# Optimization experiments

Hardware: AMD Instinct MI355X
Metric: run time of the kernel (lower is better)

## Reference

```python
import jax, jax.numpy as jnp
import numpy as np
jax.config.update("jax_enable_x64", True)

N_FFT = 512; HOP = 128; WIN = 512
LAMBDA = 2e-4      # lambda_reg (diagonal loading)
TAPS = 20          # n_frames_past
FCP_EPS = 1e-3     # fcp_epsilon


def _sqrt_hann():
    n = jnp.arange(WIN, dtype=jnp.float32)
    return jnp.sqrt(0.5 * (1.0 - jnp.cos(2.0 * jnp.pi * n / WIN)))


def _stft(x):
    # x: [B, L] float32 -> [B, n_freq, n_frames] complex64 (center=True, constant pad)
    w = _sqrt_hann()
    pad = N_FFT // 2
    xp = jnp.pad(x, ((0, 0), (pad, pad)))
    n_frames = 1 + (xp.shape[-1] - N_FFT) // HOP
    idx = jnp.arange(n_frames)[:, None] * HOP + jnp.arange(N_FFT)[None, :]
    frames = xp[:, idx] * w                      # [B, n_frames, n_fft]
    return jnp.swapaxes(jnp.fft.rfft(frames, axis=-1), -1, -2)


def _istft(spec):
    # spec: [B, n_freq, n_frames] -> [B, (n_frames-1)*HOP]  (torch.istft semantics)
    w = _sqrt_hann()
    frames = jnp.fft.irfft(jnp.swapaxes(spec, -1, -2), n=N_FFT, axis=-1) * w
    n_frames = frames.shape[1]
    Lout = (n_frames - 1) * HOP + N_FFT
    idx = jnp.arange(n_frames)[:, None] * HOP + jnp.arange(N_FFT)[None, :]
    y = jnp.zeros((frames.shape[0], Lout), frames.dtype).at[:, idx].add(frames)
    env = jnp.zeros((Lout,), frames.dtype).at[idx].add(jnp.broadcast_to(w * w, idx.shape))
    y = y / jnp.where(env > 1e-11, env, 1.0)
    pad = N_FFT // 2
    return y[:, pad:Lout - pad]


def _fcp_forward(ref_channel, mixture):
    bs, n_spk, L0 = ref_channel.shape
    n_ch = mixture.shape[1]
    ref = jnp.pad(ref_channel, ((0, 0), (0, 0), (0, N_FFT)))
    mix = jnp.pad(mixture, ((0, 0), (0, 0), (0, N_FFT)))
    sph = _stft(ref.reshape(bs * n_spk, -1))
    mxs = _stft(mix.reshape(bs * n_ch, -1))
    F_, T = sph.shape[-2], sph.shape[-1]
    sph = sph.reshape(bs, n_spk, F_, T).transpose(0, 2, 1, 3)   # [b,f,s,t]
    mxs = mxs.reshape(bs, n_ch, F_, T).transpose(0, 2, 1, 3)    # [b,f,c,t]
    # inverse power weight (fcp_weight_type=0): per (b,f,t), averaged over mics
    power = jnp.mean(mxs.real ** 2 + mxs.imag ** 2, axis=2)     # [b,f,t]
    mx = jnp.max(power, axis=(1, 2), keepdims=True)             # [b,1,1]
    inv_pow = 1.0 / (power + mx * FCP_EPS + 1e-6)               # [b,f,t]
    # Toeplitz stack: Yt[b,f,s,t,p] = sph[b,f,s, t-(TAPS-1)+p] (zero-padded past)
    padded = jnp.pad(sph, ((0, 0), (0, 0), (0, 0), (TAPS - 1, 0)))
    tidx = jnp.arange(TAPS)[:, None] + jnp.arange(T)[None, :]   # [taps, T]
    Yt = jnp.moveaxis(padded[..., tidx], -2, -1)                # [b,f,s,t,taps]
    wYt = Yt * inv_pow[:, :, None, :, None]                     # weighted copy
    R = jnp.einsum('bfstp,bfstq->bfspq', wYt, Yt.conj()) / T    # [b,f,s,taps,taps]
    P = jnp.einsum('bfstp,bfct->bfspc', wYt, mxs.conj()) / T    # [b,f,s,taps,c]
    eye = jnp.eye(TAPS, dtype=jnp.complex128)
    G = jnp.linalg.solve(R.astype(jnp.complex128) + LAMBDA * eye,
                         P.astype(jnp.complex128)).astype(Yt.dtype)
    ret = jnp.einsum('bfstp,bfspc->bfstc', Yt, G.conj())        # [b,f,s,t,c]
    spec_hat = ret.transpose(0, 2, 4, 1, 3).reshape(bs * n_spk * n_ch, F_, T)
    audio = _istft(spec_hat).reshape(bs, n_spk, n_ch, -1)[..., :L0]
    return G.conj(), audio


def setup_inputs():
    key = jax.random.key(0)
    k1, k2 = jax.random.split(key)
    ref_channel = jax.random.normal(k1, (4, 2, 64000), dtype=jnp.float32)
    mixture = jax.random.normal(k2, (4, 6, 64000), dtype=jnp.float32)
    return {"ref_channel": ref_channel, "mixture": mixture}


def reference(ref_channel, mixture):
    return _fcp_forward(ref_channel, mixture)
```

## Files before the change

### kernel.cpp

```cpp
#include <hip/hip_runtime.h>
#include <math.h>

namespace {

constexpr int NB = 4, NSPK = 2, NCHN = 6;
constexpr int LSIG = 64000;
constexpr int NFFT = 512, HOPSZ = 128, NFREQ = 257;
constexpr int NT = 505;
constexpr int TAPS = 20;
constexpr int NG = NB * NFREQ * NSPK;
constexpr int NSIG = NB * NSPK * NCHN;
constexpr float PI_F = 3.14159265358979323846f;
constexpr double LAMBDA_REG = 2e-4;
constexpr float FCP_EPS_F = 1e-3f;
constexpr int G_ELEMS = NG * TAPS * NCHN;
constexpr int NCH4 = (NT + 3) / 4;
constexpr int YPAD_N = TAPS + 2 + NT;
constexpr int NR_TILES = 55;
constexpr int NP_THREADS = 60;

constexpr size_t WS_ALIGN = 256;
constexpr size_t align_up(size_t x) { return (x + WS_ALIGN - 1) & ~(WS_ALIGN - 1); }

constexpr size_t SPH_B  = 0;
constexpr size_t SPH_SZ = (size_t)NB * NSPK * NFREQ * NT * 8;
constexpr size_t SPHT_B = align_up(SPH_B + SPH_SZ);
constexpr size_t MXS_B  = align_up(SPHT_B + SPH_SZ);
constexpr size_t MXS_SZ = (size_t)NB * NCHN * NFREQ * NT * 8;
constexpr size_t POW_B  = align_up(MXS_B + MXS_SZ);
constexpr size_t POW_SZ = (size_t)NB * NFREQ * NT * 4;
constexpr size_t MX_B   = align_up(POW_B + POW_SZ);
constexpr size_t R_B    = align_up(MX_B + (size_t)NB * 4);
constexpr size_t R_SZ   = (size_t)NG * TAPS * TAPS * 8;
constexpr size_t P_B    = align_up(R_B + R_SZ);
constexpr size_t P_SZ   = (size_t)NG * TAPS * NCHN * 8;
constexpr size_t GCT_B  = align_up(P_B + P_SZ);
constexpr size_t GCT_SZ = (size_t)NB * NSPK * TAPS * NCHN * NFREQ * 8;
constexpr size_t FRM_B  = align_up(GCT_B + GCT_SZ);

__device__ __forceinline__ int rev9(int n) { return (int)(__brev((unsigned)n) >> 23); }

__device__ __forceinline__ void fft512_quad(float2* buf, int tid, float sign) {
#pragma unroll
  for (int s = 1; s <= 9; ++s) {
    int half = 1 << (s - 1);
    int blk = tid >> (s - 1);
    int pos = tid & (half - 1);
    int i0 = (blk << s) + pos;
    int i1 = i0 + half;
    float ang = sign * 2.0f * PI_F * (float)pos / (float)(half << 1);
    float sn, cs;
    __sincosf(ang, &sn, &cs);
#pragma unroll
    for (int j = 0; j < 4; ++j) {
      float2 u = buf[j * NFFT + i0], v = buf[j * NFFT + i1];
      float2 vw = make_float2(v.x * cs - v.y * sn, v.x * sn + v.y * cs);
      buf[j * NFFT + i0] = make_float2(u.x + vw.x, u.y + vw.y);
      buf[j * NFFT + i1] = make_float2(u.x - vw.x, u.y - vw.y);
    }
    __syncthreads();
  }
}

__global__ void stft_kernel(const float* __restrict__ ref, const float* __restrict__ mix,
                            float2* __restrict__ sph, float2* __restrict__ spht,
                            float2* __restrict__ mxs) {
  __shared__ float2 buf[4 * NFFT];
  int blk = blockIdx.x;
  int sig = blk / NCH4;
  int ch = blk - sig * NCH4;
  int t0 = ch * 4;
  int nv = min(4, NT - t0);
  int tid = threadIdx.x;
  bool is_ref = sig < NB * NSPK;
  int m = is_ref ? sig : (sig - NB * NSPK);
  const float* src = is_ref ? (ref + (size_t)m * LSIG) : (mix + (size_t)m * LSIG);

  for (int n = tid; n < NFFT; n += 256) {
    float w = __sinf(PI_F * (float)n / (float)NFFT);
    int r = rev9(n);
    int g0 = t0 * HOPSZ + n - NFFT / 2;
#pragma unroll
    for (int j = 0; j < 4; ++j) {
      int gg = g0 + j * HOPSZ;
      float v = (j < nv && gg >= 0 && gg < LSIG) ? src[gg] : 0.0f;
      buf[j * NFFT + r] = make_float2(v * w, 0.0f);
    }
  }
  __syncthreads();
  fft512_quad(buf, tid, -1.0f);

  if (is_ref) {
    float2* d1 = sph + (size_t)m * NFREQ * NT;
    float2* d2 = spht + ((size_t)m * NT + t0) * NFREQ;
    for (int f = tid; f < NFREQ; f += 256) {
#pragma unroll
      for (int j = 0; j < 4; ++j) {
        if (j < nv) {
          float2 v = buf[j * NFFT + f];
          d1[(size_t)f * NT + t0 + j] = v;
          d2[(size_t)j * NFREQ + f] = v;
        }
      }
    }
  } else {
    float2* d1 = mxs + (size_t)m * NFREQ * NT;
    for (int f = tid; f < NFREQ; f += 256) {
#pragma unroll
      for (int j = 0; j < 4; ++j)
        if (j < nv) d1[(size_t)f * NT + t0 + j] = buf[j * NFFT + f];
    }
  }
}

__global__ void power_kernel(const float2* __restrict__ mxs, float* __restrict__ power) {
  int i = blockIdx.x * 256 + threadIdx.x;
  if (i >= NB * NFREQ * NT) return;
  int b = i / (NFREQ * NT);
  int r = i - b * (NFREQ * NT);
  float acc = 0.0f;
#pragma unroll
  for (int c = 0; c < NCHN; ++c) {
    float2 v = mxs[(size_t)(b * NCHN + c) * NFREQ * NT + r];
    acc += v.x * v.x + v.y * v.y;
  }
  power[i] = acc * (1.0f / (float)NCHN);
}

__global__ void max_kernel(const float* __restrict__ power, float* __restrict__ mx) {
  int b = blockIdx.x;
  const float* p = power + (size_t)b * NFREQ * NT;
  float m = 0.0f;
  for (int i = threadIdx.x; i < NFREQ * NT; i += 256) m = fmaxf(m, p[i]);
#pragma unroll
  for (int off = 32; off > 0; off >>= 1) m = fmaxf(m, __shfl_down(m, off, 64));
  __shared__ float sm[4];
  int wave = threadIdx.x >> 6, lane = threadIdx.x & 63;
  if (lane == 0) sm[wave] = m;
  __syncthreads();
  if (threadIdx.x == 0) mx[b] = fmaxf(fmaxf(sm[0], sm[1]), fmaxf(sm[2], sm[3]));
}

__global__ void rp_kernel(const float2* __restrict__ sph, const float2* __restrict__ mxs,
                          const float* __restrict__ power, const float* __restrict__ mx,
                          float2* __restrict__ R, float2* __restrict__ P) {
  __shared__ float2 Ypad[YPAD_N];
  __shared__ float2 MWsh[NCHN][NT];
  __shared__ float Wsh[NT];
  int g = blockIdx.x;
  int s = g & 1;
  int bf = g >> 1;
  int f = bf % NFREQ;
  int b = bf / NFREQ;
  int tid = threadIdx.x;

  const float2* yrow = sph + ((size_t)(b * NSPK + s) * NFREQ + f) * NT;
  const float* prow = power + ((size_t)b * NFREQ + f) * NT;
  float add = mx[b] * FCP_EPS_F + 1e-6f;
  for (int t = tid; t < NT; t += 512) Wsh[t] = 1.0f / (prow[t] + add);
  for (int i = tid; i < YPAD_N; i += 512) {
    bool in = (i >= TAPS - 1) && (i < TAPS - 1 + NT);
    Ypad[i] = in ? yrow[i - (TAPS - 1)] : make_float2(0.0f, 0.0f);
  }
  __syncthreads();
  for (int i = tid; i < NCHN * NT; i += 512) {
    int c = i / NT, t = i - c * NT;
    float2 m = mxs[((size_t)(b * NCHN + c) * NFREQ + f) * NT + t];
    float w = Wsh[t];
    MWsh[c][t] = make_float2(w * m.x, -w * m.y);
  }
  __syncthreads();

  const float invT = 1.0f / (float)NT;
  const int TQ[5] = {0, 126, 252, 378, NT};
  int wave = tid >> 6;
  int lane = tid & 63;
  bool isR = (wave < 4) && (lane < NR_TILES);
  bool isP = (wave >= 4) && (lane < NP_THREADS);

  float x00 = 0.f, y00 = 0.f, x01 = 0.f, y01 = 0.f;
  float x10 = 0.f, y10 = 0.f, x11 = 0.f, y11 = 0.f;
  int pb = 0, qb = 0, pc = 0;

  if (isR) {
    int seg = wave;
    int tlo = TQ[seg], thi = TQ[seg + 1];
    int I = (int)((sqrtf(8.0f * (float)lane + 1.0f) - 1.0f) * 0.5f);
    while ((I + 1) * (I + 2) / 2 <= lane) ++I;
    while (I * (I + 1) / 2 > lane) --I;
    int J = lane - I * (I + 1) / 2;
    pb = 2 * I; qb = 2 * J;
    float2 a0 = Ypad[pb + tlo], a1 = Ypad[pb + tlo + 1];
    float2 b0 = Ypad[qb + tlo], b1 = Ypad[qb + tlo + 1];
    for (int t = tlo; t < thi; ++t) {
      float w = Wsh[t];
      float wax0 = w * a0.x, way0 = w * a0.y;
      float wax1 = w * a1.x, way1 = w * a1.y;
      x00 = fmaf(wax0, b0.x, fmaf(way0, b0.y, x00));
      y00 = fmaf(way0, b0.x, fmaf(-wax0, b0.y, y00));
      x01 = fmaf(wax0, b1.x, fmaf(way0, b1.y, x01));
      y01 = fmaf(way0, b1.x, fmaf(-wax0, b1.y, y01));
      x10 = fmaf(wax1, b0.x, fmaf(way1, b0.y, x10));
      y10 = fmaf(way1, b0.x, fmaf(-wax1, b0.y, y10));
      x11 = fmaf(wax1, b1.x, fmaf(way1, b1.y, x11));
      y11 = fmaf(way1, b1.x, fmaf(-wax1, b1.y, y11));
      a0 = a1; a1 = Ypad[pb + 2 + t];
      b0 = b1; b1 = Ypad[qb + 2 + t];
    }
  } else if (isP) {
    int seg = wave - 4;
    int tlo = TQ[seg], thi = TQ[seg + 1];
    int ih = lane / NCHN;
    pc = lane - ih * NCHN;
    pb = 2 * ih;
    float2 a0 = Ypad[pb + tlo], a1 = Ypad[pb + tlo + 1];
    const float2* MW = &MWsh[pc][0];
    for (int t = tlo; t < thi; ++t) {
      float2 mw = MW[t];
      x00 += a0.x * mw.x - a0.y * mw.y;
      y00 += a0.x * mw.y + a0.y * mw.x;
      x10 += a1.x * mw.x - a1.y * mw.y;
      y10 += a1.x * mw.y + a1.y * mw.x;
      a0 = a1; a1 = Ypad[pb + 2 + t];
    }
  }
  __syncthreads();

  float* scratch = (float*)MWsh;
  if (isR && wave >= 1) {
    float* d = scratch + ((wave - 1) * NR_TILES + lane) * 8;
    d[0] = x00; d[1] = y00; d[2] = x01; d[3] = y01;
    d[4] = x10; d[5] = y10; d[6] = x11; d[7] = y11;
  }
  if (isP && wave >= 5) {
    float* d = scratch + 3 * NR_TILES * 8 + ((wave - 5) * NP_THREADS + lane) * 4;
    d[0] = x00; d[1] = y00; d[2] = x10; d[3] = y10;
  }
  __syncthreads();

  if (isR && wave == 0) {
#pragma unroll
    for (int sgi = 0; sgi < 3; ++sgi) {
      const float* d = scratch + (sgi * NR_TILES + lane) * 8;
      x00 += d[0]; y00 += d[1]; x01 += d[2]; y01 += d[3];
      x10 += d[4]; y10 += d[5]; x11 += d[6]; y11 += d[7];
    }
    float2* Rg = R + (size_t)g * TAPS * TAPS;
#define STORE_R(p_, q_, xx, yy)                                       \
    if ((p_) >= (q_)) {                                                \
      float rx = (xx) * invT, ry = (yy) * invT;                        \
      Rg[(p_) * TAPS + (q_)] = make_float2(rx, ry);                    \
      if ((p_) != (q_)) Rg[(q_) * TAPS + (p_)] = make_float2(rx, -ry); \
    }
    STORE_R(pb, qb, x00, y00)
    STORE_R(pb, qb + 1, x01, y01)
    STORE_R(pb + 1, qb, x10, y10)
    STORE_R(pb + 1, qb + 1, x11, y11)
#undef STORE_R
  }
  if (isP && wave == 4) {
#pragma unroll
    for (int sgi = 0; sgi < 3; ++sgi) {
      const float* d = scratch + 3 * NR_TILES * 8 + (sgi * NP_THREADS + lane) * 4;
      x00 += d[0]; y00 += d[1]; x10 += d[2]; y10 += d[3];
    }
    float2* Pg = P + (size_t)g * TAPS * NCHN;
    Pg[pb * NCHN + pc] = make_float2(x00 * invT, y00 * invT);
    Pg[(pb + 1) * NCHN + pc] = make_float2(x10 * invT, y10 * invT);
  }
}

__global__ void solve_kernel(const float2* __restrict__ R, const float2* __restrict__ P,
                             float* __restrict__ gout, float2* __restrict__ gct) {
  __shared__ double2 A[TAPS][TAPS];
  __shared__ double2 Bm[TAPS][NCHN];
  int g = blockIdx.x;
  int tid = threadIdx.x;
  int s = g & 1;
  int bf = g >> 1;
  int f = bf % NFREQ;
  int b = bf / NFREQ;
  int bs = b * NSPK + s;

  for (int i = tid; i < TAPS * TAPS; i += 64) {
    float2 r = R[(size_t)g * TAPS * TAPS + i];
    A[i / TAPS][i % TAPS] = make_double2((double)r.x, (double)r.y);
  }
  for (int i = tid; i < TAPS * NCHN; i += 64) {
    float2 p = P[(size_t)g * TAPS * NCHN + i];
    Bm[i / NCHN][i % NCHN] = make_double2((double)p.x, (double)p.y);
  }
  __syncthreads();
  if (tid < TAPS) A[tid][tid].x += LAMBDA_REG;
  __syncthreads();

  for (int k = 0; k < TAPS; ++k) {
    if (tid == 0) A[k][k].x = sqrt(A[k][k].x);
    __syncthreads();
    double d = A[k][k].x;
    if (tid > k && tid < TAPS) {
      A[tid][k].x /= d;
      A[tid][k].y /= d;
    }
    __syncthreads();
    int w = TAPS - 1 - k;
    for (int idx = tid; idx < w * w; idx += 64) {
      int i = k + 1 + idx / w;
      int j = k + 1 + idx % w;
      if (i >= j) {
        double2 a = A[i][k], bb = A[j][k];
        A[i][j].x -= a.x * bb.x + a.y * bb.y;
        A[i][j].y -= a.y * bb.x - a.x * bb.y;
      }
    }
    __syncthreads();
  }

  if (tid < NCHN) {
    int c = tid;
    for (int k = 0; k < TAPS; ++k) {
      double sx = Bm[k][c].x, sy = Bm[k][c].y;
      for (int j = 0; j < k; ++j) {
        double2 l = A[k][j], y = Bm[j][c];
        sx -= l.x * y.x - l.y * y.y;
        sy -= l.x * y.y + l.y * y.x;
      }
      double d = A[k][k].x;
      Bm[k][c] = make_double2(sx / d, sy / d);
    }
    for (int k = TAPS - 1; k >= 0; --k) {
      double sx = Bm[k][c].x, sy = Bm[k][c].y;
      for (int j = k + 1; j < TAPS; ++j) {
        double2 l = A[j][k], xv = Bm[j][c];
        sx -= l.x * xv.x + l.y * xv.y;
        sy -= l.x * xv.y - l.y * xv.x;
      }
      double d = A[k][k].x;
      Bm[k][c] = make_double2(sx / d, sy / d);
    }
  }
  __syncthreads();

  for (int i = tid; i < TAPS * NCHN; i += 64) {
    int p = i / NCHN, c = i - p * NCHN;
    double2 gv = Bm[p][c];
    float gx = (float)gv.x, gy = (float)(-gv.y);
    gout[(size_t)g * TAPS * NCHN + i] = gx;
    gct[(((size_t)bs * TAPS + p) * NCHN + c) * NFREQ + f] = make_float2(gx, gy);
  }
}

__global__ void ret_ifft_kernel(const float2* __restrict__ spht, const float2* __restrict__ gct,
                                float* __restrict__ frames) {
  __shared__ float2 buf[4 * NFFT];
  constexpr int NBLK = NSIG * NCH4;
  int bid = blockIdx.x;
  int blk = (bid & 7) * (NBLK / 8) + (bid >> 3);
  int ch = blk % NCH4;
  int sc = blk / NCH4;
  int t0 = ch * 4;
  int nv = min(4, NT - t0);
  int c = sc % NCHN;
  int bs = sc / NCHN;
  int tid = threadIdx.x;

  const float2* gbase = gct + ((size_t)bs * TAPS * NCHN + c) * NFREQ;
  const float2* ysig = spht + (size_t)bs * NT * NFREQ;
  for (int f = tid; f < NFREQ; f += 256) {
    float sx0 = 0.f, sy0 = 0.f, sx1 = 0.f, sy1 = 0.f;
    float sx2 = 0.f, sy2 = 0.f, sx3 = 0.f, sy3 = 0.f;
    float2 g1p = make_float2(0.f, 0.f), g2p = make_float2(0.f, 0.f),
           g3p = make_float2(0.f, 0.f);
#pragma unroll
    for (int k = 0; k <= TAPS + 2; ++k) {
      int u = t0 - (TAPS - 1) + k;
      float2 y = (u >= 0 && u < NT) ? ysig[(size_t)u * NFREQ + f] : make_float2(0.f, 0.f);
      float2 gc = (k < TAPS) ? gbase[(size_t)k * NCHN * NFREQ + f] : make_float2(0.f, 0.f);
      sx0 += y.x * gc.x - y.y * gc.y;   sy0 += y.x * gc.y + y.y * gc.x;
      sx1 += y.x * g1p.x - y.y * g1p.y; sy1 += y.x * g1p.y + y.y * g1p.x;
      sx2 += y.x * g2p.x - y.y * g2p.y; sy2 += y.x * g2p.y + y.y * g2p.x;
      sx3 += y.x * g3p.x - y.y * g3p.y; sy3 += y.x * g3p.y + y.y * g3p.x;
      g3p = g2p; g2p = g1p; g1p = gc;
    }
    int r = rev9(f);
    buf[r] = make_float2(sx0, sy0);
    buf[NFFT + r] = make_float2(sx1, sy1);
    buf[2 * NFFT + r] = make_float2(sx2, sy2);
    buf[3 * NFFT + r] = make_float2(sx3, sy3);
    if (f > 0 && f < NFFT / 2) {
      int r2 = rev9(NFFT - f);
      buf[r2] = make_float2(sx0, -sy0);
      buf[NFFT + r2] = make_float2(sx1, -sy1);
      buf[2 * NFFT + r2] = make_float2(sx2, -sy2);
      buf[3 * NFFT + r2] = make_float2(sx3, -sy3);
    }
  }
  __syncthreads();
  fft512_quad(buf, tid, +1.0f);

  float* frow = frames + ((size_t)sc * NT + t0) * NFFT;
  for (int n = tid; n < NFFT; n += 256) {
    float w = __sinf(PI_F * (float)n / (float)NFFT);
#pragma unroll
    for (int j = 0; j < 4; ++j)
      if (j < nv) frow[(size_t)j * NFFT + n] = buf[j * NFFT + n].x * (1.0f / (float)NFFT) * w;
  }
}

__global__ void ola_kernel(const float* __restrict__ frames, float* __restrict__ out) {
  int i = blockIdx.x * 256 + threadIdx.x;
  if (i >= NSIG * LSIG) return;
  int sig = i / LSIG;
  int l = i - sig * LSIG;
  int lp = l + NFFT / 2;
  int j0 = max(0, (lp - (NFFT - HOPSZ)) / HOPSZ);
  int j1 = min(NT - 1, lp / HOPSZ);
  float acc = 0.0f;
  for (int j = j0; j <= j1; ++j) {
    int n = lp - j * HOPSZ;
    acc += frames[((size_t)sig * NT + j) * NFFT + n];
  }
  float env;
  if (j1 - j0 == 3) {
    env = 2.0f;
  } else {
    env = 0.0f;
    for (int j = j0; j <= j1; ++j) {
      int n = lp - j * HOPSZ;
      float w = __sinf(PI_F * (float)n / (float)NFFT);
      env += w * w;
    }
    if (env <= 1e-11f) env = 1.0f;
  }
  out[(size_t)G_ELEMS + i] = acc / env;
}

}

extern "C" void kernel_launch(void* const* d_in, const int* in_sizes, int n_in,
                              void* d_out, int out_size, void* d_ws, size_t ws_size,
                              hipStream_t stream) {
  const float* ref = (const float*)d_in[0];
  const float* mix = (const float*)d_in[1];
  if (n_in >= 2 && in_sizes[0] > in_sizes[1]) {
    const float* tmp = ref; ref = mix; mix = tmp;
  }
  char* ws = (char*)d_ws;

  float2*  sph   = (float2*)(ws + SPH_B);
  float2*  spht  = (float2*)(ws + SPHT_B);
  float2*  mxs   = (float2*)(ws + MXS_B);
  float*   power = (float*)(ws + POW_B);
  float*   mx    = (float*)(ws + MX_B);
  float2*  R     = (float2*)(ws + R_B);
  float2*  P     = (float2*)(ws + P_B);
  float2*  gct   = (float2*)(ws + GCT_B);
  float*   frames= (float*)(ws + FRM_B);
  float*   out   = (float*)d_out;

  stft_kernel<<<dim3((NB * NSPK + NB * NCHN) * NCH4), dim3(256), 0, stream>>>(ref, mix, sph, spht, mxs);
  power_kernel<<<dim3((NB * NFREQ * NT + 255) / 256), dim3(256), 0, stream>>>(mxs, power);
  max_kernel<<<dim3(NB), dim3(256), 0, stream>>>(power, mx);
  rp_kernel<<<dim3(NG), dim3(512), 0, stream>>>(sph, mxs, power, mx, R, P);
  solve_kernel<<<dim3(NG), dim3(64), 0, stream>>>(R, P, out, gct);
  ret_ifft_kernel<<<dim3(NSIG * NCH4), dim3(256), 0, stream>>>(spht, gct, frames);
  ola_kernel<<<dim3((NSIG * LSIG + 255) / 256), dim3(256), 0, stream>>>(frames, out);
}
```

Measured before the change: 364.2 us.

## Fuse power and max via atomicMax; process both speakers per rp block

Merges the power and max kernels into one: each block reduces its tile and publishes the per-batch max with an atomicMax on the float bit pattern, after a memset of the max buffer. The rp kernel now handles both speakers of a (b,f) pair in one block, so the mixture weighting and inverse power are loaded and staged in shared memory once and reused for both speakers, at the cost of half as many blocks and more accumulator registers per thread. The unsigned-int atomicMax is only correct because power is non-negative.

```diff
diff --git a/kernel.cpp b/kernel.cpp
--- a/kernel.cpp
+++ b/kernel.cpp
@@ -9,6 +9,7 @@
 constexpr int NT = 505;
 constexpr int TAPS = 20;
 constexpr int NG = NB * NFREQ * NSPK;
+constexpr int NBF = NB * NFREQ;
 constexpr int NSIG = NB * NSPK * NCHN;
 constexpr float PI_F = 3.14159265358979323846f;
 constexpr double LAMBDA_REG = 2e-4;
@@ -18,6 +19,7 @@
 constexpr int YPAD_N = TAPS + 2 + NT;
 constexpr int NR_TILES = 55;
 constexpr int NP_THREADS = 60;
+constexpr int PM_BLOCKS_PER_B = (NFREQ * NT + 255) / 256;
 
 constexpr size_t WS_ALIGN = 256;
 constexpr size_t align_up(size_t x) { return (x + WS_ALIGN - 1) & ~(WS_ALIGN - 1); }
@@ -113,54 +115,55 @@
   }
 }
 
-__global__ void power_kernel(const float2* __restrict__ mxs, float* __restrict__ power) {
-  int i = blockIdx.x * 256 + threadIdx.x;
-  if (i >= NB * NFREQ * NT) return;
-  int b = i / (NFREQ * NT);
-  int r = i - b * (NFREQ * NT);
+__global__ void power_max_kernel(const float2* __restrict__ mxs, float* __restrict__ power,
+                                 unsigned int* __restrict__ mx_u) {
+  int blk = blockIdx.x;
+  int b = blk / PM_BLOCKS_PER_B;
+  int k = blk - b * PM_BLOCKS_PER_B;
+  int r = k * 256 + threadIdx.x;
   float acc = 0.0f;
-#pragma unroll
-  for (int c = 0; c < NCHN; ++c) {
-    float2 v = mxs[(size_t)(b * NCHN + c) * NFREQ * NT + r];
-    acc += v.x * v.x + v.y * v.y;
-  }
-  power[i] = acc * (1.0f / (float)NCHN);
-}
-
-__global__ void max_kernel(const float* __restrict__ power, float* __restrict__ mx) {
-  int b = blockIdx.x;
-  const float* p = power + (size_t)b * NFREQ * NT;
-  float m = 0.0f;
-  for (int i = threadIdx.x; i < NFREQ * NT; i += 256) m = fmaxf(m, p[i]);
+  if (r < NFREQ * NT) {
+#pragma unroll
+    for (int c = 0; c < NCHN; ++c) {
+      float2 v = mxs[(size_t)(b * NCHN + c) * NFREQ * NT + r];
+      acc += v.x * v.x + v.y * v.y;
+    }
+    acc *= (1.0f / (float)NCHN);
+    power[(size_t)b * NFREQ * NT + r] = acc;
+  }
+  float m = acc;
 #pragma unroll
   for (int off = 32; off > 0; off >>= 1) m = fmaxf(m, __shfl_down(m, off, 64));
   __shared__ float sm[4];
   int wave = threadIdx.x >> 6, lane = threadIdx.x & 63;
   if (lane == 0) sm[wave] = m;
   __syncthreads();
-  if (threadIdx.x == 0) mx[b] = fmaxf(fmaxf(sm[0], sm[1]), fmaxf(sm[2], sm[3]));
+  if (threadIdx.x == 0) {
+    float mm = fmaxf(fmaxf(sm[0], sm[1]), fmaxf(sm[2], sm[3]));
+    atomicMax(&mx_u[b], __float_as_uint(mm));
+  }
 }
 
 __global__ void rp_kernel(const float2* __restrict__ sph, const float2* __restrict__ mxs,
                           const float* __restrict__ power, const float* __restrict__ mx,
                           float2* __restrict__ R, float2* __restrict__ P) {
-  __shared__ float2 Ypad[YPAD_N];
+  __shared__ float2 Ypad[NSPK][YPAD_N];
   __shared__ float2 MWsh[NCHN][NT];
   __shared__ float Wsh[NT];
-  int g = blockIdx.x;
-  int s = g & 1;
-  int bf = g >> 1;
+  int bf = blockIdx.x;
   int f = bf % NFREQ;
   int b = bf / NFREQ;
   int tid = threadIdx.x;
 
-  const float2* yrow = sph + ((size_t)(b * NSPK + s) * NFREQ + f) * NT;
   const float* prow = power + ((size_t)b * NFREQ + f) * NT;
   float add = mx[b] * FCP_EPS_F + 1e-6f;
   for (int t = tid; t < NT; t += 512) Wsh[t] = 1.0f / (prow[t] + add);
-  for (int i = tid; i < YPAD_N; i += 512) {
-    bool in = (i >= TAPS - 1) && (i < TAPS - 1 + NT);
-    Ypad[i] = in ? yrow[i - (TAPS - 1)] : make_float2(0.0f, 0.0f);
+  for (int i = tid; i < NSPK * YPAD_N; i += 512) {
+    int sp = i / YPAD_N, j = i - sp * YPAD_N;
+    bool in = (j >= TAPS - 1) && (j < TAPS - 1 + NT);
+    Ypad[sp][j] = in
+        ? sph[((size_t)(b * NSPK + sp) * NFREQ + f) * NT + (j - (TAPS - 1))]
+        : make_float2(0.0f, 0.0f);
   }
   __syncthreads();
   for (int i = tid; i < NCHN * NT; i += 512) {
@@ -177,96 +180,143 @@
   int lane = tid & 63;
   bool isR = (wave < 4) && (lane < NR_TILES);
   bool isP = (wave >= 4) && (lane < NP_THREADS);
-
-  float x00 = 0.f, y00 = 0.f, x01 = 0.f, y01 = 0.f;
-  float x10 = 0.f, y10 = 0.f, x11 = 0.f, y11 = 0.f;
+  int seg = wave & 3;
+
+  float x00[2] = {0.f, 0.f}, y00[2] = {0.f, 0.f}, x01[2] = {0.f, 0.f}, y01[2] = {0.f, 0.f};
+  float x10[2] = {0.f, 0.f}, y10[2] = {0.f, 0.f}, x11[2] = {0.f, 0.f}, y11[2] = {0.f, 0.f};
   int pb = 0, qb = 0, pc = 0;
 
   if (isR) {
-    int seg = wave;
     int tlo = TQ[seg], thi = TQ[seg + 1];
     int I = (int)((sqrtf(8.0f * (float)lane + 1.0f) - 1.0f) * 0.5f);
     while ((I + 1) * (I + 2) / 2 <= lane) ++I;
     while (I * (I + 1) / 2 > lane) --I;
     int J = lane - I * (I + 1) / 2;
     pb = 2 * I; qb = 2 * J;
-    float2 a0 = Ypad[pb + tlo], a1 = Ypad[pb + tlo + 1];
-    float2 b0 = Ypad[qb + tlo], b1 = Ypad[qb + tlo + 1];
+    float2 a0s0 = Ypad[0][pb + tlo], a1s0 = Ypad[0][pb + tlo + 1];
+    float2 b0s0 = Ypad[0][qb + tlo], b1s0 = Ypad[0][qb + tlo + 1];
+    float2 a0s1 = Ypad[1][pb + tlo], a1s1 = Ypad[1][pb + tlo + 1];
+    float2 b0s1 = Ypad[1][qb + tlo], b1s1 = Ypad[1][qb + tlo + 1];
     for (int t = tlo; t < thi; ++t) {
       float w = Wsh[t];
-      float wax0 = w * a0.x, way0 = w * a0.y;
-      float wax1 = w * a1.x, way1 = w * a1.y;
-      x00 = fmaf(wax0, b0.x, fmaf(way0, b0.y, x00));
-      y00 = fmaf(way0, b0.x, fmaf(-wax0, b0.y, y00));
-      x01 = fmaf(wax0, b1.x, fmaf(way0, b1.y, x01));
-      y01 = fmaf(way0, b1.x, fmaf(-wax0, b1.y, y01));
-      x10 = fmaf(wax1, b0.x, fmaf(way1, b0.y, x10));
-      y10 = fmaf(way1, b0.x, fmaf(-wax1, b0.y, y10));
-      x11 = fmaf(wax1, b1.x, fmaf(way1, b1.y, x11));
-      y11 = fmaf(way1, b1.x, fmaf(-wax1, b1.y, y11));
-      a0 = a1; a1 = Ypad[pb + 2 + t];
-      b0 = b1; b1 = Ypad[qb + 2 + t];
+      {
+        float wax0 = w * a0s0.x, way0 = w * a0s0.y;
+        float wax1 = w * a1s0.x, way1 = w * a1s0.y;
+        x00[0] = fmaf(wax0, b0s0.x, fmaf(way0, b0s0.y, x00[0]));
+        y00[0] = fmaf(way0, b0s0.x, fmaf(-wax0, b0s0.y, y00[0]));
+        x01[0] = fmaf(wax0, b1s0.x, fmaf(way0, b1s0.y, x01[0]));
+        y01[0] = fmaf(way0, b1s0.x, fmaf(-wax0, b1s0.y, y01[0]));
+        x10[0] = fmaf(wax1, b0s0.x, fmaf(way1, b0s0.y, x10[0]));
+        y10[0] = fmaf(way1, b0s0.x, fmaf(-wax1, b0s0.y, y10[0]));
+        x11[0] = fmaf(wax1, b1s0.x, fmaf(way1, b1s0.y, x11[0]));
+        y11[0] = fmaf(way1, b1s0.x, fmaf(-wax1, b1s0.y, y11[0]));
+        a0s0 = a1s0; a1s0 = Ypad[0][pb + 2 + t];
+        b0s0 = b1s0; b1s0 = Ypad[0][qb + 2 + t];
+      }
+      {
+        float wax0 = w * a0s1.x, way0 = w * a0s1.y;
+        float wax1 = w * a1s1.x, way1 = w * a1s1.y;
+        x00[1] = fmaf(wax0, b0s1.x, fmaf(way0, b0s1.y, x00[1]));
+        y00[1] = fmaf(way0, b0s1.x, fmaf(-wax0, b0s1.y, y00[1]));
+        x01[1] = fmaf(wax0, b1s1.x, fmaf(way0, b1s1.y, x01[1]));
+        y01[1] = fmaf(way0, b1s1.x, fmaf(-wax0, b1s1.y, y01[1]));
+        x10[1] = fmaf(wax1, b0s1.x, fmaf(way1, b0s1.y, x10[1]));
+        y10[1] = fmaf(way1, b0s1.x, fmaf(-wax1, b0s1.y, y10[1]));
+        x11[1] = fmaf(wax1, b1s1.x, fmaf(way1, b1s1.y, x11[1]));
+        y11[1] = fmaf(way1, b1s1.x, fmaf(-wax1, b1s1.y, y11[1]));
+        a0s1 = a1s1; a1s1 = Ypad[1][pb + 2 + t];
+        b0s1 = b1s1; b1s1 = Ypad[1][qb + 2 + t];
+      }
     }
   } else if (isP) {
-    int seg = wave - 4;
     int tlo = TQ[seg], thi = TQ[seg + 1];
     int ih = lane / NCHN;
     pc = lane - ih * NCHN;
     pb = 2 * ih;
-    float2 a0 = Ypad[pb + tlo], a1 = Ypad[pb + tlo + 1];
+    float2 a0s0 = Ypad[0][pb + tlo], a1s0 = Ypad[0][pb + tlo + 1];
+    float2 a0s1 = Ypad[1][pb + tlo], a1s1 = Ypad[1][pb + tlo + 1];
     const float2* MW = &MWsh[pc][0];
     for (int t = tlo; t < thi; ++t) {
       float2 mw = MW[t];
-      x00 += a0.x * mw.x - a0.y * mw.y;
-      y00 += a0.x * mw.y + a0.y * mw.x;
-      x10 += a1.x * mw.x - a1.y * mw.y;
-      y10 += a1.x * mw.y + a1.y * mw.x;
-      a0 = a1; a1 = Ypad[pb + 2 + t];
+      x00[0] += a0s0.x * mw.x - a0s0.y * mw.y;
+      y00[0] += a0s0.x * mw.y + a0s0.y * mw.x;
+      x10[0] += a1s0.x * mw.x - a1s0.y * mw.y;
+      y10[0] += a1s0.x * mw.y + a1s0.y * mw.x;
+      x00[1] += a0s1.x * mw.x - a0s1.y * mw.y;
+      y00[1] += a0s1.x * mw.y + a0s1.y * mw.x;
+      x10[1] += a1s1.x * mw.x - a1s1.y * mw.y;
+      y10[1] += a1s1.x * mw.y + a1s1.y * mw.x;
+      a0s0 = a1s0; a1s0 = Ypad[0][pb + 2 + t];
+      a0s1 = a1s1; a1s1 = Ypad[1][pb + 2 + t];
     }
   }
   __syncthreads();
 
   float* scratch = (float*)MWsh;
-  if (isR && wave >= 1) {
-    float* d = scratch + ((wave - 1) * NR_TILES + lane) * 8;
-    d[0] = x00; d[1] = y00; d[2] = x01; d[3] = y01;
-    d[4] = x10; d[5] = y10; d[6] = x11; d[7] = y11;
-  }
-  if (isP && wave >= 5) {
-    float* d = scratch + 3 * NR_TILES * 8 + ((wave - 5) * NP_THREADS + lane) * 4;
-    d[0] = x00; d[1] = y00; d[2] = x10; d[3] = y10;
-  }
-  __syncthreads();
-
-  if (isR && wave == 0) {
+  if (isR && seg >= 1) {
+    float* d = scratch + ((seg - 1) * NR_TILES + lane) * 16;
+#pragma unroll
+    for (int sp = 0; sp < 2; ++sp) {
+      d[sp * 8 + 0] = x00[sp]; d[sp * 8 + 1] = y00[sp];
+      d[sp * 8 + 2] = x01[sp]; d[sp * 8 + 3] = y01[sp];
+      d[sp * 8 + 4] = x10[sp]; d[sp * 8 + 5] = y10[sp];
+      d[sp * 8 + 6] = x11[sp]; d[sp * 8 + 7] = y11[sp];
+    }
+  }
+  if (isP && seg >= 1) {
+    float* d = scratch + 3 * NR_TILES * 16 + ((seg - 1) * NP_THREADS + lane) * 8;
+#pragma unroll
+    for (int sp = 0; sp < 2; ++sp) {
+      d[sp * 4 + 0] = x00[sp]; d[sp * 4 + 1] = y00[sp];
+      d[sp * 4 + 2] = x10[sp]; d[sp * 4 + 3] = y10[sp];
+    }
+  }
+  __syncthreads();
+
+  if (isR && seg == 0) {
 #pragma unroll
     for (int sgi = 0; sgi < 3; ++sgi) {
-      const float* d = scratch + (sgi * NR_TILES + lane) * 8;
-      x00 += d[0]; y00 += d[1]; x01 += d[2]; y01 += d[3];
-      x10 += d[4]; y10 += d[5]; x11 += d[6]; y11 += d[7];
-    }
-    float2* Rg = R + (size_t)g * TAPS * TAPS;
+      const float* d = scratch + (sgi * NR_TILES + lane) * 16;
+#pragma unroll
+      for (int sp = 0; sp < 2; ++sp) {
+        x00[sp] += d[sp * 8 + 0]; y00[sp] += d[sp * 8 + 1];
+        x01[sp] += d[sp * 8 + 2]; y01[sp] += d[sp * 8 + 3];
+        x10[sp] += d[sp * 8 + 4]; y10[sp] += d[sp * 8 + 5];
+        x11[sp] += d[sp * 8 + 6]; y11[sp] += d[sp * 8 + 7];
+      }
+    }
+#pragma unroll
+    for (int sp = 0; sp < 2; ++sp) {
+      float2* Rg = R + (size_t)(bf * NSPK + sp) * TAPS * TAPS;
 #define STORE_R(p_, q_, xx, yy)                                       \
-    if ((p_) >= (q_)) {                                                \
-      float rx = (xx) * invT, ry = (yy) * invT;                        \
-      Rg[(p_) * TAPS + (q_)] = make_float2(rx, ry);                    \
-      if ((p_) != (q_)) Rg[(q_) * TAPS + (p_)] = make_float2(rx, -ry); \
-    }
-    STORE_R(pb, qb, x00, y00)
-    STORE_R(pb, qb + 1, x01, y01)
-    STORE_R(pb + 1, qb, x10, y10)
-    STORE_R(pb + 1, qb + 1, x11, y11)
+      if ((p_) >= (q_)) {                                              \
+        float rx = (xx) * invT, ry = (yy) * invT;                      \
+        Rg[(p_) * TAPS + (q_)] = make_float2(rx, ry);                  \
+        if ((p_) != (q_)) Rg[(q_) * TAPS + (p_)] = make_float2(rx, -ry); \
+      }
+      STORE_R(pb, qb, x00[sp], y00[sp])
+      STORE_R(pb, qb + 1, x01[sp], y01[sp])
+      STORE_R(pb + 1, qb, x10[sp], y10[sp])
+      STORE_R(pb + 1, qb + 1, x11[sp], y11[sp])
 #undef STORE_R
-  }
-  if (isP && wave == 4) {
+    }
+  }
+  if (isP && seg == 0) {
 #pragma unroll
     for (int sgi = 0; sgi < 3; ++sgi) {
-      const float* d = scratch + 3 * NR_TILES * 8 + (sgi * NP_THREADS + lane) * 4;
-      x00 += d[0]; y00 += d[1]; x10 += d[2]; y10 += d[3];
-    }
-    float2* Pg = P + (size_t)g * TAPS * NCHN;
-    Pg[pb * NCHN + pc] = make_float2(x00 * invT, y00 * invT);
-    Pg[(pb + 1) * NCHN + pc] = make_float2(x10 * invT, y10 * invT);
+      const float* d = scratch + 3 * NR_TILES * 16 + (sgi * NP_THREADS + lane) * 8;
+#pragma unroll
+      for (int sp = 0; sp < 2; ++sp) {
+        x00[sp] += d[sp * 4 + 0]; y00[sp] += d[sp * 4 + 1];
+        x10[sp] += d[sp * 4 + 2]; y10[sp] += d[sp * 4 + 3];
+      }
+    }
+#pragma unroll
+    for (int sp = 0; sp < 2; ++sp) {
+      float2* Pg = P + (size_t)(bf * NSPK + sp) * TAPS * NCHN;
+      Pg[pb * NCHN + pc] = make_float2(x00[sp] * invT, y00[sp] * invT);
+      Pg[(pb + 1) * NCHN + pc] = make_float2(x10[sp] * invT, y10[sp] * invT);
+    }
   }
 }
 
@@ -458,10 +508,11 @@
   float*   frames= (float*)(ws + FRM_B);
   float*   out   = (float*)d_out;
 
+  hipMemsetAsync(mx, 0, NB * sizeof(float), stream);
   stft_kernel<<<dim3((NB * NSPK + NB * NCHN) * NCH4), dim3(256), 0, stream>>>(ref, mix, sph, spht, mxs);
-  power_kernel<<<dim3((NB * NFREQ * NT + 255) / 256), dim3(256), 0, stream>>>(mxs, power);
-  max_kernel<<<dim3(NB), dim3(256), 0, stream>>>(power, mx);
-  rp_kernel<<<dim3(NG), dim3(512), 0, stream>>>(sph, mxs, power, mx, R, P);
+  power_max_kernel<<<dim3(NB * PM_BLOCKS_PER_B), dim3(256), 0, stream>>>(
+      mxs, power, (unsigned int*)mx);
+  rp_kernel<<<dim3(NBF), dim3(512), 0, stream>>>(sph, mxs, power, mx, R, P);
   solve_kernel<<<dim3(NG), dim3(64), 0, stream>>>(R, P, out, gct);
   ret_ifft_kernel<<<dim3(NSIG * NCH4), dim3(256), 0, stream>>>(spht, gct, frames);
   ola_kernel<<<dim3((NSIG * LSIG + 255) / 256), dim3(256), 0, stream>>>(frames, out);
```

Result: faster. 319.3 us (-12.3%).
